# Kernel tuning notes

Measured on AMD Instinct MI355X. Metric: run time of the kernel, lower is better.

Reference implementation:

```python
import jax, jax.numpy as jnp
import numpy as np

N, C, H, W = 8, 21, 512, 512
POWER = 1
EPS = 1e-8

def setup_inputs() -> dict:
    key = jax.random.key(0)
    k1, k2 = jax.random.split(key)
    inp = jax.random.normal(k1, (N, C, H, W), dtype=jnp.float32)
    tgt = jax.random.normal(k2, (N, C, H, W), dtype=jnp.float32)
    return {"input": inp, "target": tgt}

def reference(input, target):
    n, c, h, w = input.shape
    # target.argmax(1) -> one-hot mask (to_one_hot with clamp; argmax already in [0, c-1])
    labels = jnp.argmax(target, axis=1)                      # [n, h, w]
    ymask = jax.nn.one_hot(labels, c, axis=1, dtype=input.dtype)  # [n, c, h, w]

    log_p = jax.nn.log_softmax(input, axis=1)
    p = jax.nn.softmax(input, axis=1)

    # lambda_mat is None -> zf_dict: lamb[i][j] = 0.5 for all i, j
    lamb = jnp.full((c, c), 0.5, dtype=input.dtype)

    # Per-class pixel counts n_i and pairwise sums S[i, j] = sum(p[:, i] * ymask[:, j])
    counts = ymask.sum(axis=(0, 2, 3))                       # [c]
    S = jnp.einsum('nihw,njhw->ij', p, ymask)                # [c, c]

    safe_counts = jnp.where(counts > 0, counts, 1.0)
    diag = jnp.diagonal(S)                                   # S[i, i]
    # mcc.sum() for pair (i, j) = S[i,i]/n_i - S[i,j]/n_j
    mcc_sum = diag[:, None] / safe_counts[:, None] - S / safe_counts[None, :]

    term = -lamb * jnp.log((0.5 * mcc_sum + 0.5) ** POWER + EPS)
    valid = (counts[:, None] > 0) & (counts[None, :] > 0) & (~jnp.eye(c, dtype=bool))
    lossd = jnp.where(valid, term, 0.0).sum()

    # weight is None -> ymask1 == ymask
    logpy = (log_p * ymask).sum(axis=1)                      # [n, h, w]
    loss = -logpy.mean()
    return loss + lossd
```

## Files before the change

### kernel.cpp

```cpp
#include <hip/hip_runtime.h>

#define BLOCK 512
#define GRID 4096

namespace {
constexpr int C = 21;
constexpr int HW = 512 * 512;
constexpr int NPIX = 8 * HW;
constexpr float EPS = 1e-8f;
constexpr int WS_CNT = C * C;
constexpr int WS_LOGP = C * C + C;
constexpr int ACC_USED = C * C + C + 1;
constexpr int ACC_STRIDE = 464;
constexpr int MAX_COPIES = 64;
}

__global__ __launch_bounds__(BLOCK) void wce_main(const float* __restrict__ inp,
                                                  const float* __restrict__ tgt,
                                                  float* __restrict__ acc,
                                                  int copy_mask) {
    __shared__ float sS[C * C];
    __shared__ float sCnt[C];
    __shared__ float sRed[BLOCK / 64];

    const int tid = threadIdx.x;
    for (int i = tid; i < C * C; i += BLOCK) sS[i] = 0.f;
    if (tid < C) sCnt[tid] = 0.f;
    __syncthreads();

    const int px = blockIdx.x * BLOCK + tid;
    const int n = px >> 18;
    const int hw = px & (HW - 1);
    const size_t base = (size_t)n * (size_t)(C * HW) + (size_t)hw;
    const float* __restrict__ tp = tgt + base;
    const float* __restrict__ ip = inp + base;

    float bv = tp[0];
    int lab = 0;
#pragma unroll
    for (int c = 1; c < C; ++c) {
        const float v = tp[c * HW];
        if (v > bv) { bv = v; lab = c; }
    }

    float x[C];
#pragma unroll
    for (int c = 0; c < C; ++c) x[c] = ip[c * HW];
    float m = x[0];
#pragma unroll
    for (int c = 1; c < C; ++c) m = fmaxf(m, x[c]);

    float xlab = x[0];
#pragma unroll
    for (int c = 1; c < C; ++c) if (lab == c) xlab = x[c];

    float s = 0.f;
#pragma unroll
    for (int c = 0; c < C; ++c) { x[c] = __expf(x[c] - m); s += x[c]; }

    const float logpy = xlab - m - __logf(s);

    const float inv = 1.f / s;
#pragma unroll
    for (int c = 0; c < C; ++c) unsafeAtomicAdd(&sS[c * C + lab], x[c] * inv);
    unsafeAtomicAdd(&sCnt[lab], 1.f);

    float lp = logpy;
#pragma unroll
    for (int off = 32; off > 0; off >>= 1) lp += __shfl_down(lp, off);
    if ((tid & 63) == 0) sRed[tid >> 6] = lp;
    __syncthreads();

    float* __restrict__ a = acc + (size_t)(blockIdx.x & copy_mask) * ACC_STRIDE;
    for (int i = tid; i < C * C; i += BLOCK) unsafeAtomicAdd(&a[i], sS[i]);
    if (tid < C) unsafeAtomicAdd(&a[WS_CNT + tid], sCnt[tid]);
    if (tid == 0) {
        float t = 0.f;
#pragma unroll
        for (int wv = 0; wv < BLOCK / 64; ++wv) t += sRed[wv];
        unsafeAtomicAdd(&a[WS_LOGP], t);
    }
}

__global__ void wce_final(const float* __restrict__ acc, float* __restrict__ out,
                          int copies) {
    __shared__ float tot[ACC_USED];
    __shared__ float red[8];
    const int tid = threadIdx.x;

    for (int i = tid; i < ACC_USED; i += 512) {
        float s = 0.f;
        for (int k = 0; k < copies; ++k) s += acc[(size_t)k * ACC_STRIDE + i];
        tot[i] = s;
    }
    __syncthreads();

    float partial = 0.f;
    if (tid < C * C) {
        const int i = tid / C;
        const int j = tid - i * C;
        if (i != j) {
            const float ci = tot[WS_CNT + i], cj = tot[WS_CNT + j];
            if (ci > 0.f && cj > 0.f) {
                const float mcc = tot[i * C + i] / ci - tot[i * C + j] / cj;
                partial = -0.5f * __logf(0.5f * mcc + 0.5f + EPS);
            }
        }
    }
#pragma unroll
    for (int off = 32; off > 0; off >>= 1) partial += __shfl_down(partial, off);
    if ((tid & 63) == 0) red[tid >> 6] = partial;
    __syncthreads();

    if (tid == 0) {
        float lossd = 0.f;
#pragma unroll
        for (int wv = 0; wv < 8; ++wv) lossd += red[wv];
        const float loss = -tot[WS_LOGP] / (float)NPIX;
        out[0] = loss + lossd;
    }
}

extern "C" void kernel_launch(void* const* d_in, const int* in_sizes, int n_in,
                              void* d_out, int out_size, void* d_ws, size_t ws_size,
                              hipStream_t stream) {
    const float* inp = (const float*)d_in[0];
    const float* tgt = (const float*)d_in[1];
    float* acc = (float*)d_ws;
    float* out = (float*)d_out;

    int copies = 1;
    const size_t per = (size_t)ACC_STRIDE * sizeof(float);
    while (copies * 2 <= MAX_COPIES && (size_t)(copies * 2) * per <= ws_size) copies *= 2;

    hipMemsetAsync(acc, 0, (size_t)copies * per, stream);
    wce_main<<<GRID, BLOCK, 0, stream>>>(inp, tgt, acc, copies - 1);
    wce_final<<<1, 512, 0, stream>>>(acc, out, copies);
}
```

Measured before the change: 272.5 us.

## Process 16 pixels per thread with float4 loads and two-pass softmax without max

Each block now covers a 4096-pixel tile, and each thread handles four float4 vectors. The channels are streamed twice: the first pass accumulates the exp-sum and the label logit, and the second pass reloads the input, recomputes exp, and adds normalized probabilities into shared memory. This removes the per-thread 21-register channel array and the max subtraction, and it widens loads. The cost is a second read of the input tensor, possibly served from cache, and a risk of overflow because the max is no longer subtracted.

```diff
diff --git a/kernel.cpp b/kernel.cpp
--- a/kernel.cpp
+++ b/kernel.cpp
@@ -1,12 +1,15 @@
 #include <hip/hip_runtime.h>
 
-#define BLOCK 512
-#define GRID 4096
+#define BLOCK 256
+#define GRID 512
 
 namespace {
 constexpr int C = 21;
 constexpr int HW = 512 * 512;
 constexpr int NPIX = 8 * HW;
+constexpr int PTILE = 4096;
+constexpr int K = PTILE / (BLOCK * 4);
+constexpr int CH4 = HW / 4;
 constexpr float EPS = 1e-8f;
 constexpr int WS_CNT = C * C;
 constexpr int WS_LOGP = C * C + C;
@@ -28,44 +31,83 @@
     if (tid < C) sCnt[tid] = 0.f;
     __syncthreads();
 
-    const int px = blockIdx.x * BLOCK + tid;
-    const int n = px >> 18;
-    const int hw = px & (HW - 1);
-    const size_t base = (size_t)n * (size_t)(C * HW) + (size_t)hw;
-    const float* __restrict__ tp = tgt + base;
-    const float* __restrict__ ip = inp + base;
+    const int px0 = blockIdx.x * PTILE;
+    const int n = px0 >> 18;
+    const int hw = px0 & (HW - 1);
+    const float4* __restrict__ tp =
+        reinterpret_cast<const float4*>(tgt + (size_t)n * (size_t)(C * HW) + hw);
+    const float4* __restrict__ ip =
+        reinterpret_cast<const float4*>(inp + (size_t)n * (size_t)(C * HW) + hw);
 
-    float bv = tp[0];
-    int lab = 0;
+    int4 lab[K];
+    float4 bv[K];
 #pragma unroll
+    for (int k = 0; k < K; ++k) {
+        bv[k] = tp[k * BLOCK + tid];
+        lab[k] = make_int4(0, 0, 0, 0);
+    }
     for (int c = 1; c < C; ++c) {
-        const float v = tp[c * HW];
-        if (v > bv) { bv = v; lab = c; }
+#pragma unroll
+        for (int k = 0; k < K; ++k) {
+            const float4 t = tp[c * CH4 + k * BLOCK + tid];
+            if (t.x > bv[k].x) { bv[k].x = t.x; lab[k].x = c; }
+            if (t.y > bv[k].y) { bv[k].y = t.y; lab[k].y = c; }
+            if (t.z > bv[k].z) { bv[k].z = t.z; lab[k].z = c; }
+            if (t.w > bv[k].w) { bv[k].w = t.w; lab[k].w = c; }
+        }
     }
 
-    float x[C];
+    float4 s[K], xl[K];
 #pragma unroll
-    for (int c = 0; c < C; ++c) x[c] = ip[c * HW];
-    float m = x[0];
+    for (int k = 0; k < K; ++k) {
+        s[k] = make_float4(0.f, 0.f, 0.f, 0.f);
+        xl[k] = make_float4(0.f, 0.f, 0.f, 0.f);
+    }
+    for (int c = 0; c < C; ++c) {
 #pragma unroll
-    for (int c = 1; c < C; ++c) m = fmaxf(m, x[c]);
+        for (int k = 0; k < K; ++k) {
+            const float4 v = ip[c * CH4 + k * BLOCK + tid];
+            s[k].x += __expf(v.x);
+            s[k].y += __expf(v.y);
+            s[k].z += __expf(v.z);
+            s[k].w += __expf(v.w);
+            if (lab[k].x == c) xl[k].x = v.x;
+            if (lab[k].y == c) xl[k].y = v.y;
+            if (lab[k].z == c) xl[k].z = v.z;
+            if (lab[k].w == c) xl[k].w = v.w;
+        }
+    }
 
-    float xlab = x[0];
+    float lp = 0.f;
+    float4 is[K];
 #pragma unroll
-    for (int c = 1; c < C; ++c) if (lab == c) xlab = x[c];
+    for (int k = 0; k < K; ++k) {
+        lp += (xl[k].x - __logf(s[k].x)) + (xl[k].y - __logf(s[k].y))
+            + (xl[k].z - __logf(s[k].z)) + (xl[k].w - __logf(s[k].w));
+        is[k].x = 1.f / s[k].x;
+        is[k].y = 1.f / s[k].y;
+        is[k].z = 1.f / s[k].z;
+        is[k].w = 1.f / s[k].w;
+    }
 
-    float s = 0.f;
+    for (int c = 0; c < C; ++c) {
 #pragma unroll
-    for (int c = 0; c < C; ++c) { x[c] = __expf(x[c] - m); s += x[c]; }
+        for (int k = 0; k < K; ++k) {
+            const float4 v = ip[c * CH4 + k * BLOCK + tid];
+            unsafeAtomicAdd(&sS[c * C + lab[k].x], __expf(v.x) * is[k].x);
+            unsafeAtomicAdd(&sS[c * C + lab[k].y], __expf(v.y) * is[k].y);
+            unsafeAtomicAdd(&sS[c * C + lab[k].z], __expf(v.z) * is[k].z);
+            unsafeAtomicAdd(&sS[c * C + lab[k].w], __expf(v.w) * is[k].w);
+        }
+    }
+#pragma unroll
+    for (int k = 0; k < K; ++k) {
+        unsafeAtomicAdd(&sCnt[lab[k].x], 1.f);
+        unsafeAtomicAdd(&sCnt[lab[k].y], 1.f);
+        unsafeAtomicAdd(&sCnt[lab[k].z], 1.f);
+        unsafeAtomicAdd(&sCnt[lab[k].w], 1.f);
+    }
 
-    const float logpy = xlab - m - __logf(s);
-
-    const float inv = 1.f / s;
-#pragma unroll
-    for (int c = 0; c < C; ++c) unsafeAtomicAdd(&sS[c * C + lab], x[c] * inv);
-    unsafeAtomicAdd(&sCnt[lab], 1.f);
-
-    float lp = logpy;
 #pragma unroll
     for (int off = 32; off > 0; off >>= 1) lp += __shfl_down(lp, off);
     if ((tid & 63) == 0) sRed[tid >> 6] = lp;
@@ -75,10 +117,10 @@
     for (int i = tid; i < C * C; i += BLOCK) unsafeAtomicAdd(&a[i], sS[i]);
     if (tid < C) unsafeAtomicAdd(&a[WS_CNT + tid], sCnt[tid]);
     if (tid == 0) {
-        float t = 0.f;
+        float tt = 0.f;
 #pragma unroll
-        for (int wv = 0; wv < BLOCK / 64; ++wv) t += sRed[wv];
-        unsafeAtomicAdd(&a[WS_LOGP], t);
+        for (int wv = 0; wv < BLOCK / 64; ++wv) tt += sRed[wv];
+        unsafeAtomicAdd(&a[WS_LOGP], tt);
     }
 }
 
```

Result: slower. 309.7 us (+13.7%).

## Stream channels with float4 double-buffered sweeps, four pixels per thread

Applied to the files above, without the earlier changes.

Each thread now handles four consecutive pixels through float4 loads and walks the 21 channels in a double-buffered sweep, instead of holding all channels in registers. There are three sweeps: argmax over the target, exp-sum plus gather of the labelled logit, and a re-read of the input to recompute the probabilities for the shared-memory atomics. The max subtraction is dropped from the softmax, and the block layout changes to 1024 threads and 512 blocks, with a barrier after every channel step. The aim is wider, better-coalesced loads and lower register pressure, at the cost of reading the input twice, extra barriers, and overflow risk on large logits.

```diff
diff --git a/kernel.cpp b/kernel.cpp
--- a/kernel.cpp
+++ b/kernel.cpp
@@ -1,12 +1,14 @@
 #include <hip/hip_runtime.h>
 
-#define BLOCK 512
-#define GRID 4096
+#define BLOCK 1024
+#define GRID 512
 
 namespace {
 constexpr int C = 21;
 constexpr int HW = 512 * 512;
 constexpr int NPIX = 8 * HW;
+constexpr int PTILE = BLOCK * 4;
+constexpr int CH4 = HW / 4;
 constexpr float EPS = 1e-8f;
 constexpr int WS_CNT = C * C;
 constexpr int WS_LOGP = C * C + C;
@@ -15,10 +17,21 @@
 constexpr int MAX_COPIES = 64;
 }
 
-__global__ __launch_bounds__(BLOCK) void wce_main(const float* __restrict__ inp,
-                                                  const float* __restrict__ tgt,
-                                                  float* __restrict__ acc,
-                                                  int copy_mask) {
+#define SWEEP_STEP(PTR, BODY)                                            \
+    {                                                                    \
+        float4 v = (c & 1) ? buf1 : buf0;                                \
+        if (c + 2 < C) {                                                 \
+            if (c & 1) buf1 = (PTR)[(c + 2) * CH4 + tid];                \
+            else       buf0 = (PTR)[(c + 2) * CH4 + tid];                \
+        }                                                                \
+        BODY                                                             \
+        __builtin_amdgcn_s_barrier();                                    \
+    }
+
+__global__ __launch_bounds__(BLOCK, 8) void wce_main(const float* __restrict__ inp,
+                                                     const float* __restrict__ tgt,
+                                                     float* __restrict__ acc,
+                                                     int copy_mask) {
     __shared__ float sS[C * C];
     __shared__ float sCnt[C];
     __shared__ float sRed[BLOCK / 64];
@@ -28,44 +41,56 @@
     if (tid < C) sCnt[tid] = 0.f;
     __syncthreads();
 
-    const int px = blockIdx.x * BLOCK + tid;
-    const int n = px >> 18;
-    const int hw = px & (HW - 1);
-    const size_t base = (size_t)n * (size_t)(C * HW) + (size_t)hw;
-    const float* __restrict__ tp = tgt + base;
-    const float* __restrict__ ip = inp + base;
+    const int px0 = blockIdx.x * PTILE;
+    const int n = px0 >> 18;
+    const int hw = px0 & (HW - 1);
+    const float4* __restrict__ tp =
+        reinterpret_cast<const float4*>(tgt + (size_t)n * (size_t)(C * HW) + hw);
+    const float4* __restrict__ ip =
+        reinterpret_cast<const float4*>(inp + (size_t)n * (size_t)(C * HW) + hw);
 
-    float bv = tp[0];
-    int lab = 0;
+    float4 buf0 = tp[tid];
+    float4 buf1 = tp[CH4 + tid];
+    float4 bv = make_float4(-3.4e38f, -3.4e38f, -3.4e38f, -3.4e38f);
+    int4 lab = make_int4(0, 0, 0, 0);
 #pragma unroll
-    for (int c = 1; c < C; ++c) {
-        const float v = tp[c * HW];
-        if (v > bv) { bv = v; lab = c; }
-    }
+    for (int c = 0; c < C; ++c) SWEEP_STEP(tp, {
+        if (v.x > bv.x) { bv.x = v.x; lab.x = c; }
+        if (v.y > bv.y) { bv.y = v.y; lab.y = c; }
+        if (v.z > bv.z) { bv.z = v.z; lab.z = c; }
+        if (v.w > bv.w) { bv.w = v.w; lab.w = c; }
+    })
 
-    float x[C];
+    buf0 = ip[tid];
+    buf1 = ip[CH4 + tid];
+    float4 s = make_float4(0.f, 0.f, 0.f, 0.f);
+    float4 xl = make_float4(0.f, 0.f, 0.f, 0.f);
 #pragma unroll
-    for (int c = 0; c < C; ++c) x[c] = ip[c * HW];
-    float m = x[0];
+    for (int c = 0; c < C; ++c) SWEEP_STEP(ip, {
+        s.x += __expf(v.x); if (lab.x == c) xl.x = v.x;
+        s.y += __expf(v.y); if (lab.y == c) xl.y = v.y;
+        s.z += __expf(v.z); if (lab.z == c) xl.z = v.z;
+        s.w += __expf(v.w); if (lab.w == c) xl.w = v.w;
+    })
+
+    float lp = (xl.x - __logf(s.x)) + (xl.y - __logf(s.y))
+             + (xl.z - __logf(s.z)) + (xl.w - __logf(s.w));
+    const float4 is = make_float4(1.f / s.x, 1.f / s.y, 1.f / s.z, 1.f / s.w);
+
+    buf0 = ip[tid];
+    buf1 = ip[CH4 + tid];
 #pragma unroll
-    for (int c = 1; c < C; ++c) m = fmaxf(m, x[c]);
+    for (int c = 0; c < C; ++c) SWEEP_STEP(ip, {
+        unsafeAtomicAdd(&sS[c * C + lab.x], __expf(v.x) * is.x);
+        unsafeAtomicAdd(&sS[c * C + lab.y], __expf(v.y) * is.y);
+        unsafeAtomicAdd(&sS[c * C + lab.z], __expf(v.z) * is.z);
+        unsafeAtomicAdd(&sS[c * C + lab.w], __expf(v.w) * is.w);
+    })
+    unsafeAtomicAdd(&sCnt[lab.x], 1.f);
+    unsafeAtomicAdd(&sCnt[lab.y], 1.f);
+    unsafeAtomicAdd(&sCnt[lab.z], 1.f);
+    unsafeAtomicAdd(&sCnt[lab.w], 1.f);
 
-    float xlab = x[0];
-#pragma unroll
-    for (int c = 1; c < C; ++c) if (lab == c) xlab = x[c];
-
-    float s = 0.f;
-#pragma unroll
-    for (int c = 0; c < C; ++c) { x[c] = __expf(x[c] - m); s += x[c]; }
-
-    const float logpy = xlab - m - __logf(s);
-
-    const float inv = 1.f / s;
-#pragma unroll
-    for (int c = 0; c < C; ++c) unsafeAtomicAdd(&sS[c * C + lab], x[c] * inv);
-    unsafeAtomicAdd(&sCnt[lab], 1.f);
-
-    float lp = logpy;
 #pragma unroll
     for (int off = 32; off > 0; off >>= 1) lp += __shfl_down(lp, off);
     if ((tid & 63) == 0) sRed[tid >> 6] = lp;
@@ -75,10 +100,10 @@
     for (int i = tid; i < C * C; i += BLOCK) unsafeAtomicAdd(&a[i], sS[i]);
     if (tid < C) unsafeAtomicAdd(&a[WS_CNT + tid], sCnt[tid]);
     if (tid == 0) {
-        float t = 0.f;
+        float tt = 0.f;
 #pragma unroll
-        for (int wv = 0; wv < BLOCK / 64; ++wv) t += sRed[wv];
-        unsafeAtomicAdd(&a[WS_LOGP], t);
+        for (int wv = 0; wv < BLOCK / 64; ++wv) tt += sRed[wv];
+        unsafeAtomicAdd(&a[WS_LOGP], tt);
     }
 }
 
```

Measured after the change: 342.6 us. +25.7%, slower.
